# Performance work log

Measured on AMD Instinct MI355X. Metric: run time of the kernel, lower is better.

The kernel has to match this reference:

```python
import jax, jax.numpy as jnp
import numpy as np

N_NODES = 50000
N_EDGES = 640000
NODE_DIM = 16
HIDDEN = 128
LATENT = 64
MAX_NODES = 100
NUM_GRAPHS = 256


def _xavier(key, fan_in, fan_out):
    bound = np.sqrt(6.0 / (fan_in + fan_out)).astype(np.float32)
    return jax.random.uniform(key, (fan_in, fan_out), jnp.float32, -bound, bound)


def setup_inputs() -> dict:
    key = jax.random.key(0)
    ks = jax.random.split(key, 16)
    inp = {
        "x": jax.random.normal(ks[0], (N_NODES, NODE_DIM), jnp.float32),
        "edge_index": jax.random.randint(ks[1], (2, N_EDGES), 0, N_NODES, jnp.int64),
        "batch": jnp.sort(jax.random.randint(ks[2], (N_NODES,), 0, NUM_GRAPHS, jnp.int64)),
        "eps": jax.random.normal(ks[3], (NUM_GRAPHS, LATENT), jnp.float32),
        # conv1 MLP
        "w1a": _xavier(ks[4], NODE_DIM, HIDDEN), "b1a": jnp.zeros((HIDDEN,), jnp.float32),
        "w1b": _xavier(ks[5], HIDDEN, HIDDEN), "b1b": jnp.zeros((HIDDEN,), jnp.float32),
        # conv2 MLP
        "w2a": _xavier(ks[6], HIDDEN, HIDDEN), "b2a": jnp.zeros((HIDDEN,), jnp.float32),
        "w2b": _xavier(ks[7], HIDDEN, HIDDEN), "b2b": jnp.zeros((HIDDEN,), jnp.float32),
        # heads
        "wmu": _xavier(ks[8], HIDDEN, LATENT), "bmu": jnp.zeros((LATENT,), jnp.float32),
        "wlv": _xavier(ks[9], HIDDEN, LATENT), "blv": jnp.zeros((LATENT,), jnp.float32),
        # decoder
        "wd1": _xavier(ks[10], LATENT, HIDDEN), "bd1": jnp.zeros((HIDDEN,), jnp.float32),
        "wd2": _xavier(ks[11], HIDDEN, HIDDEN), "bd2": jnp.zeros((HIDDEN,), jnp.float32),
        "wn": _xavier(ks[12], HIDDEN, MAX_NODES * NODE_DIM), "bn": jnp.zeros((MAX_NODES * NODE_DIM,), jnp.float32),
        "we": _xavier(ks[13], HIDDEN, MAX_NODES * MAX_NODES), "be": jnp.zeros((MAX_NODES * MAX_NODES,), jnp.float32),
    }
    return inp


def _gin(x, src, dst, wa, ba, wb, bb):
    # GIN with eps=0: MLP(x + sum_{j->i} x_j)
    agg = jax.ops.segment_sum(x[src], dst, num_segments=N_NODES) + x
    h = jax.nn.relu(agg @ wa + ba)
    return h @ wb + bb


def reference(x, edge_index, batch, eps,
              w1a, b1a, w1b, b1b, w2a, b2a, w2b, b2b,
              wmu, bmu, wlv, blv, wd1, bd1, wd2, bd2, wn, bn, we, be):
    src, dst = edge_index[0], edge_index[1]
    # encode
    h = jax.nn.relu(_gin(x, src, dst, w1a, b1a, w1b, b1b))
    h = jax.nn.relu(_gin(h, src, dst, w2a, b2a, w2b, b2b))
    summed = jax.ops.segment_sum(h, batch, num_segments=NUM_GRAPHS)
    counts = jax.ops.segment_sum(jnp.ones((N_NODES,), h.dtype), batch, num_segments=NUM_GRAPHS)
    pooled = summed / jnp.maximum(counts, 1.0)[:, None]
    mu = pooled @ wmu + bmu
    logvar = jnp.clip(pooled @ wlv + blv, -5.0, 5.0)
    # reparameterize
    z = mu + eps * jnp.exp(0.5 * logvar)
    # decode
    hd = jax.nn.relu(z @ wd1 + bd1) @ wd2 + bd2
    node_features = jax.nn.softmax((hd @ wn + bn).reshape(NUM_GRAPHS, MAX_NODES, NODE_DIM), axis=-1)
    adj = (hd @ we + be).reshape(NUM_GRAPHS, MAX_NODES, MAX_NODES)
    adj = (adj + jnp.swapaxes(adj, -1, -2)) * 0.5
    eye = jnp.eye(MAX_NODES, dtype=bool)
    adj = jnp.where(eye[None], -10.0, adj)
    adj = jnp.clip(adj, -10.0, 10.0)
    return adj, node_features, mu, logvar
```

## Files before the change

### kernel.cpp

```cpp
#include <hip/hip_runtime.h>
#include <hip/hip_bf16.h>

#define N_NODES   50000
#define N_EDGES   640000
#define NODE_DIM  16
#define HIDDEN    128
#define LATENT    64
#define MAX_NODES 100
#define NUM_GRAPHS 256

typedef unsigned short ushort_t;
typedef unsigned int   uint_t;
typedef short  short8 __attribute__((ext_vector_type(8)));
typedef float  f32x4  __attribute__((ext_vector_type(4)));

__device__ __forceinline__ float bf2f(ushort_t u) {
    return __uint_as_float(((uint_t)u) << 16);
}
__device__ __forceinline__ ushort_t f2bf(float f) {
    const uint_t u = __float_as_uint(f);
    return (ushort_t)((u + 0x7fffu + ((u >> 16) & 1u)) >> 16);
}

__device__ __forceinline__ void mfma_acc(f32x4& acc, short8 a, short8 b) {
    asm volatile("v_mfma_f32_16x16x32_bf16 %0, %1, %2, %0"
                 : "+v"(acc) : "v"(a), "v"(b));
}
__device__ __forceinline__ void mfma_hazard_wait() {
    asm volatile("s_nop 7\n\ts_nop 7");
}

__global__ void degree_kernel(const int* __restrict__ dst, int* __restrict__ deg) {
    const int i0 = (blockIdx.x * blockDim.x + threadIdx.x) * 4;
    if (i0 + 4 <= N_EDGES) {
        const int4 d = *(const int4*)&dst[i0];
        atomicAdd(&deg[d.x], 1);
        atomicAdd(&deg[d.y], 1);
        atomicAdd(&deg[d.z], 1);
        atomicAdd(&deg[d.w], 1);
    }
}

__global__ void blockscan_kernel(const int* __restrict__ deg,
                                 int* __restrict__ row_start,
                                 int* __restrict__ blocksum) {
    __shared__ int s_wave[16];
    const int tid  = threadIdx.x;
    const int lane = tid & 63;
    const int wid  = tid >> 6;
    const int idx  = blockIdx.x * 1024 + tid;

    const int v = (idx < N_NODES) ? deg[idx] : 0;
    int x = v;
    #pragma unroll
    for (int o = 1; o < 64; o <<= 1) {
        const int y = __shfl_up(x, o);
        if (lane >= o) x += y;
    }
    if (lane == 63) s_wave[wid] = x;
    __syncthreads();
    if (tid == 0) {
        int run = 0;
        #pragma unroll
        for (int w = 0; w < 16; ++w) { const int t = s_wave[w]; s_wave[w] = run; run += t; }
        blocksum[blockIdx.x] = run;
    }
    __syncthreads();
    if (idx < N_NODES) row_start[idx] = s_wave[wid] + x - v;
}

__global__ void scan_fixup_kernel(int* __restrict__ row_start,
                                  int* __restrict__ cursor,
                                  const int* __restrict__ blocksum) {
    __shared__ int s_off;
    const int bid = blockIdx.x;
    const int tid = threadIdx.x;
    if (tid < 64) {
        int v = (tid < bid) ? blocksum[tid] : 0;
        #pragma unroll
        for (int o = 32; o > 0; o >>= 1) v += __shfl_down(v, o);
        if (tid == 0) s_off = v;
    }
    __syncthreads();
    const int idx = bid * 1024 + tid;
    if (idx < N_NODES) {
        const int r = row_start[idx] + s_off;
        row_start[idx] = r;
        cursor[idx] = r;
    }
    if (bid == 0 && tid == 0) row_start[N_NODES] = N_EDGES;
}

__global__ void csr_fill_kernel(const int* __restrict__ src,
                                const int* __restrict__ dst,
                                int* __restrict__ cursor,
                                int* __restrict__ nbr) {
    const int i0 = (blockIdx.x * blockDim.x + threadIdx.x) * 4;
    if (i0 + 4 <= N_EDGES) {
        const int4 d = *(const int4*)&dst[i0];
        const int4 s = *(const int4*)&src[i0];
        const int p0 = atomicAdd(&cursor[d.x], 1);
        const int p1 = atomicAdd(&cursor[d.y], 1);
        const int p2 = atomicAdd(&cursor[d.z], 1);
        const int p3 = atomicAdd(&cursor[d.w], 1);
        nbr[p0] = s.x; nbr[p1] = s.y; nbr[p2] = s.z; nbr[p3] = s.w;
    }
}

__global__ void pack_w3_kernel(const float* __restrict__ wA, ushort_t* __restrict__ oA,
                               const float* __restrict__ wB, ushort_t* __restrict__ oB,
                               const float* __restrict__ wC, ushort_t* __restrict__ oC) {
    const int gid = blockIdx.x * blockDim.x + threadIdx.x;
    const int sel = gid >> 14;
    const int idx = gid & 16383;
    const float* w = (sel == 0) ? wA : (sel == 1) ? wB : wC;
    ushort_t* out  = (sel == 0) ? oA : (sel == 1) ? oB : oC;
    const int j    = idx & 7;
    const int lane = (idx >> 3) & 63;
    const int kb   = (idx >> 9) & 3;
    const int nt   = idx >> 11;
    const int k = kb * 32 + ((lane >> 4) << 3) + j;
    const int n = (nt << 4) + (lane & 15);
    out[idx] = f2bf(w[k * HIDDEN + n]);
}

__global__ void gin1_fused_kernel(const float* __restrict__ in,
                                  const int* __restrict__ row_start,
                                  const int* __restrict__ nbr,
                                  const float* __restrict__ wa, const float* __restrict__ ba,
                                  const ushort_t* __restrict__ wpkb, const float* __restrict__ bb,
                                  ushort_t* __restrict__ out) {
    __shared__ float s_in[16][NODE_DIM + 1];
    __shared__ __align__(16) ushort_t s_mid[16][HIDDEN + 8];
    const int tid = threadIdx.x;
    const int n0  = blockIdx.x * 16;

    {
        const int grp = tid >> 4;
        const int k   = tid & 15;
        #pragma unroll
        for (int half = 0; half < 2; ++half) {
            const int i = grp + half * 8;
            const int n = n0 + i;
            const int beg = row_start[n], end = row_start[n + 1];
            float a0 = in[(long)n * NODE_DIM + k], a1 = 0.f, a2 = 0.f, a3 = 0.f;
            int p = beg;
            for (; p + 4 <= end; p += 4) {
                const int e0 = nbr[p], e1 = nbr[p + 1], e2 = nbr[p + 2], e3 = nbr[p + 3];
                a0 += in[(long)e0 * NODE_DIM + k];
                a1 += in[(long)e1 * NODE_DIM + k];
                a2 += in[(long)e2 * NODE_DIM + k];
                a3 += in[(long)e3 * NODE_DIM + k];
            }
            for (; p < end; ++p) a0 += in[(long)nbr[p] * NODE_DIM + k];
            s_in[i][k] = (a0 + a1) + (a2 + a3);
        }
    }
    __syncthreads();

    {
        const int dq = tid & 31;  const int d0 = dq * 4;
        const int iq = tid >> 5;  const int i0 = iq * 4;
        float acc[4][4];
        const float4 bv = *(const float4*)&ba[d0];
        #pragma unroll
        for (int j = 0; j < 4; ++j) {
            acc[j][0] = bv.x; acc[j][1] = bv.y; acc[j][2] = bv.z; acc[j][3] = bv.w;
        }
        for (int k = 0; k < NODE_DIM; ++k) {
            const float4 w = *(const float4*)&wa[k * HIDDEN + d0];
            #pragma unroll
            for (int j = 0; j < 4; ++j) {
                const float a = s_in[i0 + j][k];
                acc[j][0] += a * w.x; acc[j][1] += a * w.y;
                acc[j][2] += a * w.z; acc[j][3] += a * w.w;
            }
        }
        #pragma unroll
        for (int j = 0; j < 4; ++j) {
            ushort4 v;
            v.x = f2bf(fmaxf(acc[j][0], 0.f)); v.y = f2bf(fmaxf(acc[j][1], 0.f));
            v.z = f2bf(fmaxf(acc[j][2], 0.f)); v.w = f2bf(fmaxf(acc[j][3], 0.f));
            *(ushort4*)&s_mid[i0 + j][d0] = v;
        }
    }
    __syncthreads();

    {
        const int lane = tid & 63;
        const int wv   = tid >> 6;
        short8 afr[4];
        #pragma unroll
        for (int kb = 0; kb < 4; ++kb)
            afr[kb] = *(const short8*)&s_mid[lane & 15][kb * 32 + ((lane >> 4) << 3)];
        const int col = lane & 15;
        const int r0  = (lane >> 4) << 2;
        #pragma unroll
        for (int t = 0; t < 4; ++t) {
            const int nt = wv * 4 + t;
            short8 bfr[4];
            #pragma unroll
            for (int kb = 0; kb < 4; ++kb)
                bfr[kb] = *(const short8*)&wpkb[(((nt << 2) | kb) << 9) + (lane << 3)];
            f32x4 acc = {0.f, 0.f, 0.f, 0.f};
            #pragma unroll
            for (int kb = 0; kb < 4; ++kb) mfma_acc(acc, afr[kb], bfr[kb]);
            mfma_hazard_wait();
            const float bias = bb[nt * 16 + col];
            #pragma unroll
            for (int r = 0; r < 4; ++r)
                out[(long)(n0 + r0 + r) * HIDDEN + nt * 16 + col] =
                    f2bf(fmaxf(acc[r] + bias, 0.f));
        }
    }
}

__global__ void gin2_fused_kernel(const ushort_t* __restrict__ in,
                                  const int* __restrict__ row_start,
                                  const int* __restrict__ nbr,
                                  const ushort_t* __restrict__ wpka, const float* __restrict__ ba,
                                  const ushort_t* __restrict__ wpkb, const float* __restrict__ bb,
                                  float* __restrict__ out) {
    __shared__ __align__(16) ushort_t s_in[16][HIDDEN + 8];
    __shared__ __align__(16) ushort_t s_mid[16][HIDDEN + 8];
    const int tid  = threadIdx.x;
    const int lane = tid & 63;
    const int wv   = tid >> 6;
    const int n0   = blockIdx.x * 16;

    {
        const int d2 = lane * 2;
        #pragma unroll
        for (int t = 0; t < 8; ++t) {
            const int i = wv * 8 + t;
            const int n = n0 + i;
            const int beg = row_start[n], end = row_start[n + 1];
            const uint_t sv = *(const uint_t*)&in[(long)n * HIDDEN + d2];
            float ax[8], ay[8];
            ax[0] = bf2f(sv & 0xffffu); ay[0] = bf2f(sv >> 16);
            #pragma unroll
            for (int q = 1; q < 8; ++q) { ax[q] = 0.f; ay[q] = 0.f; }
            int p = beg;
            for (; p + 8 <= end; p += 8) {
                uint_t v[8];
                #pragma unroll
                for (int q = 0; q < 8; ++q)
                    v[q] = *(const uint_t*)&in[(long)nbr[p + q] * HIDDEN + d2];
                #pragma unroll
                for (int q = 0; q < 8; ++q) {
                    ax[q] += bf2f(v[q] & 0xffffu); ay[q] += bf2f(v[q] >> 16);
                }
            }
            for (; p + 2 <= end; p += 2) {
                const uint_t v0 = *(const uint_t*)&in[(long)nbr[p]     * HIDDEN + d2];
                const uint_t v1 = *(const uint_t*)&in[(long)nbr[p + 1] * HIDDEN + d2];
                ax[0] += bf2f(v0 & 0xffffu); ay[0] += bf2f(v0 >> 16);
                ax[1] += bf2f(v1 & 0xffffu); ay[1] += bf2f(v1 >> 16);
            }
            if (p < end) {
                const uint_t v0 = *(const uint_t*)&in[(long)nbr[p] * HIDDEN + d2];
                ax[0] += bf2f(v0 & 0xffffu); ay[0] += bf2f(v0 >> 16);
            }
            const float rx = ((ax[0] + ax[1]) + (ax[2] + ax[3])) + ((ax[4] + ax[5]) + (ax[6] + ax[7]));
            const float ry = ((ay[0] + ay[1]) + (ay[2] + ay[3])) + ((ay[4] + ay[5]) + (ay[6] + ay[7]));
            const uint_t packed = (uint_t)f2bf(rx) | ((uint_t)f2bf(ry) << 16);
            *(uint_t*)&s_in[i][d2] = packed;
        }
    }
    __syncthreads();

    const int col = lane & 15;
    const int r0  = (lane >> 4) << 2;

    {
        short8 afr[4];
        #pragma unroll
        for (int kb = 0; kb < 4; ++kb)
            afr[kb] = *(const short8*)&s_in[lane & 15][kb * 32 + ((lane >> 4) << 3)];
        #pragma unroll
        for (int t = 0; t < 4; ++t) {
            const int nt = wv * 4 + t;
            short8 bfr[4];
            #pragma unroll
            for (int kb = 0; kb < 4; ++kb)
                bfr[kb] = *(const short8*)&wpka[(((nt << 2) | kb) << 9) + (lane << 3)];
            f32x4 acc = {0.f, 0.f, 0.f, 0.f};
            #pragma unroll
            for (int kb = 0; kb < 4; ++kb) mfma_acc(acc, afr[kb], bfr[kb]);
            mfma_hazard_wait();
            const float bias = ba[nt * 16 + col];
            #pragma unroll
            for (int r = 0; r < 4; ++r)
                s_mid[r0 + r][nt * 16 + col] = f2bf(fmaxf(acc[r] + bias, 0.f));
        }
    }
    __syncthreads();

    {
        short8 afr[4];
        #pragma unroll
        for (int kb = 0; kb < 4; ++kb)
            afr[kb] = *(const short8*)&s_mid[lane & 15][kb * 32 + ((lane >> 4) << 3)];
        #pragma unroll
        for (int t = 0; t < 4; ++t) {
            const int nt = wv * 4 + t;
            short8 bfr[4];
            #pragma unroll
            for (int kb = 0; kb < 4; ++kb)
                bfr[kb] = *(const short8*)&wpkb[(((nt << 2) | kb) << 9) + (lane << 3)];
            f32x4 acc = {0.f, 0.f, 0.f, 0.f};
            #pragma unroll
            for (int kb = 0; kb < 4; ++kb) mfma_acc(acc, afr[kb], bfr[kb]);
            mfma_hazard_wait();
            const float bias = bb[nt * 16 + col];
            #pragma unroll
            for (int r = 0; r < 4; ++r)
                out[(long)(n0 + r0 + r) * HIDDEN + nt * 16 + col] =
                    fmaxf(acc[r] + bias, 0.f);
        }
    }
}

__global__ void pool_kernel(const float* __restrict__ h,
                            const int* __restrict__ batch,
                            float* __restrict__ summed,
                            float* __restrict__ counts) {
    const int NPB = 32;
    const int n0 = blockIdx.x * NPB;
    if (n0 >= N_NODES) return;
    const int nend = min(n0 + NPB, N_NODES);
    const int d = threadIdx.x;

    int cur = batch[n0];
    float acc = 0.f;
    int cnt = 0;
    for (int n = n0; n < nend; ++n) {
        const int g = batch[n];
        if (g != cur) {
            atomicAdd(&summed[cur * HIDDEN + d], acc);
            if (d == 0) atomicAdd(&counts[cur], (float)cnt);
            acc = 0.f; cnt = 0; cur = g;
        }
        acc += h[(long)n * HIDDEN + d];
        ++cnt;
    }
    atomicAdd(&summed[cur * HIDDEN + d], acc);
    if (d == 0) atomicAdd(&counts[cur], (float)cnt);
}

__global__ void head_kernel(const float* __restrict__ summed,
                            const float* __restrict__ counts,
                            const float* __restrict__ eps,
                            const float* __restrict__ wmu, const float* __restrict__ bmu,
                            const float* __restrict__ wlv, const float* __restrict__ blv,
                            const float* __restrict__ wd1, const float* __restrict__ bd1,
                            const float* __restrict__ wd2, const float* __restrict__ bd2,
                            float* __restrict__ out_mu, float* __restrict__ out_lv,
                            float* __restrict__ hd) {
    const int g = blockIdx.x;
    const int d = threadIdx.x;
    __shared__ float s_pool[HIDDEN];
    __shared__ float s_z[LATENT];
    __shared__ float s_h1[HIDDEN];

    const float cnt = fmaxf(counts[g], 1.f);
    s_pool[d] = summed[g * HIDDEN + d] / cnt;
    __syncthreads();

    if (d < LATENT) {
        float m = bmu[d], lv = blv[d];
        for (int k = 0; k < HIDDEN; ++k) {
            const float p = s_pool[k];
            m  += p * wmu[k * LATENT + d];
            lv += p * wlv[k * LATENT + d];
        }
        lv = fminf(fmaxf(lv, -5.f), 5.f);
        out_mu[g * LATENT + d] = m;
        out_lv[g * LATENT + d] = lv;
        s_z[d] = m + eps[g * LATENT + d] * expf(0.5f * lv);
    }
    __syncthreads();
    {
        float a = bd1[d];
        for (int k = 0; k < LATENT; ++k) a += s_z[k] * wd1[k * HIDDEN + d];
        s_h1[d] = fmaxf(a, 0.f);
    }
    __syncthreads();
    {
        float a = bd2[d];
        for (int k = 0; k < HIDDEN; ++k) a += s_h1[k] * wd2[k * HIDDEN + d];
        hd[g * HIDDEN + d] = a;
    }
}

#define ADJ_BLOCKS 40
__global__ void decoder_gemm2_kernel(const float* __restrict__ hd,
                                     const float* __restrict__ we, const float* __restrict__ be,
                                     float* __restrict__ raw_adj,
                                     const float* __restrict__ wn, const float* __restrict__ bn,
                                     float* __restrict__ raw_nf) {
    const int GB = 16;
    const int g0 = blockIdx.y * GB;
    const bool is_adj = (blockIdx.x < ADJ_BLOCKS);
    const float* W    = is_adj ? we : wn;
    const float* bias = is_adj ? be : bn;
    float* raw        = is_adj ? raw_adj : raw_nf;
    const int N       = is_adj ? (MAX_NODES * MAX_NODES) : (MAX_NODES * NODE_DIM);
    const int o = (is_adj ? blockIdx.x : blockIdx.x - ADJ_BLOCKS) * blockDim.x + threadIdx.x;

    __shared__ float s_hd[GB][HIDDEN];
    for (int idx = threadIdx.x; idx < GB * HIDDEN; idx += blockDim.x) {
        const int g = idx >> 7;
        const int k = idx & 127;
        s_hd[g][k] = hd[(long)(g0 + g) * HIDDEN + k];
    }
    __syncthreads();
    if (o >= N) return;

    float acc[GB];
    const float bv = bias[o];
    #pragma unroll
    for (int g = 0; g < GB; ++g) acc[g] = bv;

    for (int k = 0; k < HIDDEN; ++k) {
        const float w = W[(long)k * N + o];
        #pragma unroll
        for (int g = 0; g < GB; ++g) acc[g] += s_hd[g][k] * w;
    }
    #pragma unroll
    for (int g = 0; g < GB; ++g)
        raw[(long)(g0 + g) * N + o] = acc[g];
}

__global__ void epilogue_kernel(const float* __restrict__ raw_adj,
                                float* __restrict__ out_adj,
                                const float* __restrict__ raw_nf,
                                float* __restrict__ out_nf) {
    const int tid = threadIdx.x;
    if (blockIdx.x < NUM_GRAPHS) {
        const int g = blockIdx.x;
        __shared__ float s_a[MAX_NODES * MAX_NODES];
        const float* r = raw_adj + (long)g * MAX_NODES * MAX_NODES;
        for (int o = tid; o < MAX_NODES * MAX_NODES; o += blockDim.x) s_a[o] = r[o];
        __syncthreads();
        float* w = out_adj + (long)g * MAX_NODES * MAX_NODES;
        for (int o = tid; o < MAX_NODES * MAX_NODES; o += blockDim.x) {
            const int i = o / MAX_NODES;
            const int j = o - i * MAX_NODES;
            float v;
            if (i == j) v = -10.f;
            else        v = fminf(fmaxf(0.5f * (s_a[o] + s_a[j * MAX_NODES + i]), -10.f), 10.f);
            w[o] = v;
        }
    } else {
        const int idx = (blockIdx.x - NUM_GRAPHS) * blockDim.x + tid;
        if (idx >= NUM_GRAPHS * MAX_NODES) return;
        const float* r = raw_nf + (long)idx * NODE_DIM;
        float mx = -1e30f;
        #pragma unroll
        for (int d = 0; d < NODE_DIM; ++d) mx = fmaxf(mx, r[d]);
        float e[NODE_DIM];
        float s = 0.f;
        #pragma unroll
        for (int d = 0; d < NODE_DIM; ++d) { e[d] = expf(r[d] - mx); s += e[d]; }
        const float inv = 1.f / s;
        float* w = out_nf + (long)idx * NODE_DIM;
        #pragma unroll
        for (int d = 0; d < NODE_DIM; ++d) w[d] = e[d] * inv;
    }
}

extern "C" void kernel_launch(void* const* d_in, const int* in_sizes, int n_in,
                              void* d_out, int out_size, void* d_ws, size_t ws_size,
                              hipStream_t stream) {
    const float* x    = (const float*)d_in[0];
    const int*   edge = (const int*)d_in[1];
    const int*   src  = edge;
    const int*   dst  = edge + N_EDGES;
    const int*   batch = (const int*)d_in[2];
    const float* eps  = (const float*)d_in[3];
    const float* w1a = (const float*)d_in[4],  *b1a = (const float*)d_in[5];
    const float* w1b = (const float*)d_in[6],  *b1b = (const float*)d_in[7];
    const float* w2a = (const float*)d_in[8],  *b2a = (const float*)d_in[9];
    const float* w2b = (const float*)d_in[10], *b2b = (const float*)d_in[11];
    const float* wmu = (const float*)d_in[12], *bmu = (const float*)d_in[13];
    const float* wlv = (const float*)d_in[14], *blv = (const float*)d_in[15];
    const float* wd1 = (const float*)d_in[16], *bd1 = (const float*)d_in[17];
    const float* wd2 = (const float*)d_in[18], *bd2 = (const float*)d_in[19];
    const float* wn  = (const float*)d_in[20], *bn  = (const float*)d_in[21];
    const float* we  = (const float*)d_in[22], *be  = (const float*)d_in[23];

    float* out = (float*)d_out;
    float* out_adj = out;
    float* out_nf  = out + (long)NUM_GRAPHS * MAX_NODES * MAX_NODES;
    float* out_mu  = out_nf + (long)NUM_GRAPHS * MAX_NODES * NODE_DIM;
    float* out_lv  = out_mu + NUM_GRAPHS * LATENT;

    float* ws = (float*)d_ws;
    ushort_t* h1 = (ushort_t*)ws;
    float* h2     = ws + 3200000;
    float* summed = h2 + (long)N_NODES * HIDDEN;
    float* counts = summed + NUM_GRAPHS * HIDDEN;
    float* hd     = counts + NUM_GRAPHS;
    int*   deg       = (int*)(hd + NUM_GRAPHS * HIDDEN);
    int*   row_start = deg + N_NODES;
    int*   cursor    = row_start + N_NODES + 1;
    int*   nbr       = cursor + N_NODES;
    int*   blocksum  = nbr + N_EDGES;
    ushort_t* wpk1b = (ushort_t*)(((uintptr_t)(blocksum + 64) + 15) & ~(uintptr_t)15);
    ushort_t* wpk2a = wpk1b + HIDDEN * HIDDEN;
    ushort_t* wpk2b = wpk2a + HIDDEN * HIDDEN;
    float* raw_adj = (float*)h1;
    float* raw_nf  = (float*)h1 + (long)NUM_GRAPHS * MAX_NODES * MAX_NODES;

    hipMemsetAsync(deg, 0, sizeof(int) * N_NODES, stream);
    degree_kernel<<<N_EDGES / 4 / 256, 256, 0, stream>>>(dst, deg);
    blockscan_kernel<<<(N_NODES + 1023) / 1024, 1024, 0, stream>>>(deg, row_start, blocksum);
    scan_fixup_kernel<<<(N_NODES + 1023) / 1024, 1024, 0, stream>>>(row_start, cursor, blocksum);
    csr_fill_kernel<<<N_EDGES / 4 / 256, 256, 0, stream>>>(src, dst, cursor, nbr);
    pack_w3_kernel<<<192, 256, 0, stream>>>(w1b, wpk1b, w2a, wpk2a, w2b, wpk2b);

    gin1_fused_kernel<<<N_NODES / 16, 128, 0, stream>>>(x, row_start, nbr,
                                                        w1a, b1a, wpk1b, b1b, h1);
    gin2_fused_kernel<<<N_NODES / 16, 128, 0, stream>>>(h1, row_start, nbr,
                                                        wpk2a, b2a, wpk2b, b2b, h2);

    hipMemsetAsync(summed, 0, sizeof(float) * (NUM_GRAPHS * HIDDEN + NUM_GRAPHS), stream);
    pool_kernel<<<(N_NODES + 31) / 32, 128, 0, stream>>>(h2, batch, summed, counts);

    head_kernel<<<NUM_GRAPHS, 128, 0, stream>>>(summed, counts, eps,
                                                wmu, bmu, wlv, blv,
                                                wd1, bd1, wd2, bd2,
                                                out_mu, out_lv, hd);

    {
        dim3 grid(ADJ_BLOCKS + 7, NUM_GRAPHS / 16);
        decoder_gemm2_kernel<<<grid, 256, 0, stream>>>(hd, we, be, raw_adj,
                                                       wn, bn, raw_nf);
    }

    epilogue_kernel<<<NUM_GRAPHS + 50, 512, 0, stream>>>(raw_adj, out_adj,
                                                         raw_nf, out_nf);
}
```

Measured before the change: 214.6 us.

## Register-tile decoder GEMM over 4 outputs and 8 graphs per thread

Restructures the decoder output GEMM so each thread computes a 4-output by 8-graph tile using float4 weight loads and float4 stores. Each block now covers 32 graphs instead of 16, which halves how many times the large adjacency weight matrix is streamed from memory. Shared-memory reads of the hidden vector are uniform within a wavefront, so they broadcast. The cost is half as many blocks and more registers per thread, which lowers the parallelism available to hide latency.

```diff
diff --git a/kernel.cpp b/kernel.cpp
--- a/kernel.cpp
+++ b/kernel.cpp
@@ -393,43 +393,48 @@
     }
 }
 
+#define GB2 32
 #define ADJ_BLOCKS 40
 __global__ void decoder_gemm2_kernel(const float* __restrict__ hd,
                                      const float* __restrict__ we, const float* __restrict__ be,
                                      float* __restrict__ raw_adj,
                                      const float* __restrict__ wn, const float* __restrict__ bn,
                                      float* __restrict__ raw_nf) {
-    const int GB = 16;
-    const int g0 = blockIdx.y * GB;
+    const int g0 = blockIdx.y * GB2;
     const bool is_adj = (blockIdx.x < ADJ_BLOCKS);
     const float* W    = is_adj ? we : wn;
     const float* bias = is_adj ? be : bn;
     float* raw        = is_adj ? raw_adj : raw_nf;
     const int N       = is_adj ? (MAX_NODES * MAX_NODES) : (MAX_NODES * NODE_DIM);
-    const int o = (is_adj ? blockIdx.x : blockIdx.x - ADJ_BLOCKS) * blockDim.x + threadIdx.x;
-
-    __shared__ float s_hd[GB][HIDDEN];
-    for (int idx = threadIdx.x; idx < GB * HIDDEN; idx += blockDim.x) {
-        const int g = idx >> 7;
-        const int k = idx & 127;
-        s_hd[g][k] = hd[(long)(g0 + g) * HIDDEN + k];
-    }
-    __syncthreads();
-    if (o >= N) return;
-
-    float acc[GB];
-    const float bv = bias[o];
+    const int bx      = is_adj ? blockIdx.x : blockIdx.x - ADJ_BLOCKS;
+    const int cg = threadIdx.x & 63;
+    const int gg = threadIdx.x >> 6;
+    const int o0 = bx * 256 + cg * 4;
+
+    __shared__ float s_hd[GB2][HIDDEN];
+    for (int idx = threadIdx.x; idx < GB2 * HIDDEN; idx += 256) {
+        s_hd[idx >> 7][idx & 127] = hd[(long)(g0 + (idx >> 7)) * HIDDEN + (idx & 127)];
+    }
+    __syncthreads();
+    if (o0 >= N) return;
+
+    float4 acc[8];
+    const float4 bv = *(const float4*)&bias[o0];
     #pragma unroll
-    for (int g = 0; g < GB; ++g) acc[g] = bv;
+    for (int j = 0; j < 8; ++j) acc[j] = bv;
 
     for (int k = 0; k < HIDDEN; ++k) {
-        const float w = W[(long)k * N + o];
-        #pragma unroll
-        for (int g = 0; g < GB; ++g) acc[g] += s_hd[g][k] * w;
+        const float4 w = *(const float4*)&W[(long)k * N + o0];
+        #pragma unroll
+        for (int j = 0; j < 8; ++j) {
+            const float a = s_hd[gg * 8 + j][k];
+            acc[j].x += a * w.x; acc[j].y += a * w.y;
+            acc[j].z += a * w.z; acc[j].w += a * w.w;
+        }
     }
     #pragma unroll
-    for (int g = 0; g < GB; ++g)
-        raw[(long)(g0 + g) * N + o] = acc[g];
+    for (int j = 0; j < 8; ++j)
+        *(float4*)&raw[(long)(g0 + gg * 8 + j) * N + o0] = acc[j];
 }
 
 __global__ void epilogue_kernel(const float* __restrict__ raw_adj,
@@ -534,7 +539,7 @@
                                                 out_mu, out_lv, hd);
 
     {
-        dim3 grid(ADJ_BLOCKS + 7, NUM_GRAPHS / 16);
+        dim3 grid(ADJ_BLOCKS + 7, NUM_GRAPHS / GB2);
         decoder_gemm2_kernel<<<grid, 256, 0, stream>>>(hd, we, be, raw_adj,
                                                        wn, bn, raw_nf);
     }
```

Result: no change. 218.5 us (+1.8%).
